# Kernel optimization log

Hardware: AMD Instinct MI355X
Metric: run time of the kernel (lower is better)

The kernel has to match this reference:

```python
import jax, jax.numpy as jnp
import numpy as np

B, N, M, C1, C2, H = 16, 4096, 1024, 256, 512, 256
SE_C = max(1, int(H / 24.0))  # 10
BN_EPS = 1e-5

def _bn(x, g, b):
    # training-mode BatchNorm over (B, n) per channel; x: [B, C, n]
    mean = jnp.mean(x, axis=(0, 2), keepdims=True)
    var = jnp.mean((x - mean) ** 2, axis=(0, 2), keepdims=True)  # biased var (torch)
    return (x - mean) * jax.lax.rsqrt(var + BN_EPS) * g[None, :, None] + b[None, :, None]

def _swish(x):
    return x * jax.nn.sigmoid(x)

def setup_inputs() -> dict:
    key = jax.random.key(0)
    ks = jax.random.split(key, 12)
    d = {
        "unknown": jax.random.normal(ks[0], (B, N, 3), jnp.float32),
        "known": jax.random.normal(ks[1], (B, M, 3), jnp.float32),
        "unknow_feats": jax.random.normal(ks[2], (B, C1, N), jnp.float32),
        "known_feats": jax.random.normal(ks[3], (B, C2, M), jnp.float32),
        # conv1 (C1+C2 -> H), no bias (bn)
        "W1": jax.random.normal(ks[4], (H, C1 + C2), jnp.float32) * (1.0 / np.sqrt(C1 + C2)),
        "g1": jnp.ones((H,), jnp.float32),
        "b1": jnp.zeros((H,), jnp.float32),
        # SE block (1x1 convs with bias, no pooling in this impl)
        "se_rw": jax.random.normal(ks[5], (SE_C, H), jnp.float32) * (1.0 / np.sqrt(H)),
        "se_rb": jnp.zeros((SE_C,), jnp.float32),
        "se_ew": jax.random.normal(ks[6], (H, SE_C), jnp.float32) * (1.0 / np.sqrt(SE_C)),
        "se_eb": jnp.zeros((H,), jnp.float32),
        # conv2 (H -> H), no bias
        "W2": jax.random.normal(ks[7], (H, H), jnp.float32) * (1.0 / np.sqrt(H)),
        "g2": jnp.ones((H,), jnp.float32),
        "b2": jnp.zeros((H,), jnp.float32),
    }
    return d

def reference(unknown, known, unknow_feats, known_feats,
              W1, g1, b1, se_rw, se_rb, se_ew, se_eb, W2, g2, b2):
    # three_nn: squared distances of each unknown point to all known points
    d2 = jnp.sum((unknown[:, :, None, :] - known[:, None, :, :]) ** 2, axis=-1)  # [B,N,M]
    neg_d, idx = jax.lax.top_k(-d2, 3)  # 3 smallest
    dist = -neg_d                                       # [B,N,3]
    dist_recip = 1.0 / (dist + 1e-8)
    weight = dist_recip / jnp.sum(dist_recip, axis=2, keepdims=True)  # [B,N,3]
    # three_interpolate: gather known_feats at idx, inverse-distance weighted sum
    gathered = jnp.take_along_axis(known_feats[:, :, None, :], idx[:, None, :, :], axis=3)  # [B,C2,N,3]
    interp = jnp.sum(gathered * weight[:, None, :, :], axis=-1)  # [B,C2,N]
    x = jnp.concatenate([interp, unknow_feats], axis=1)  # [B,C1+C2,N]
    # conv1 (1x1) + BN + SE
    h = jnp.einsum('oc,bcn->bon', W1, x)
    h = _bn(h, g1, b1)
    s = jnp.einsum('oc,bcn->bon', se_rw, h) + se_rb[None, :, None]
    s = _swish(s)
    s = jnp.einsum('oc,bcn->bon', se_ew, s) + se_eb[None, :, None]
    h = jax.nn.sigmoid(s) * h
    # conv2 (1x1) + BN + ReLU
    h = jnp.einsum('oc,bcn->bon', W2, h)
    h = _bn(h, g2, b2)
    return jax.nn.relu(h)  # [B, H, N]
```

## Files before the change

kernel.cpp:

```cpp
#include <hip/hip_runtime.h>
#include <math.h>

#define B_ 16
#define N_ 4096
#define M_ 1024
#define C1_ 256
#define C2_ 512
#define H_ 256
#define SEC_ 10
#define OC_ 8
#define BN_EPS 1e-5f

typedef _Float16 f16;
typedef f16 f16x8 __attribute__((ext_vector_type(8)));
typedef f16 f16x4 __attribute__((ext_vector_type(4)));
typedef f16 f16x2 __attribute__((ext_vector_type(2)));
typedef float f32x4 __attribute__((ext_vector_type(4)));

__global__ __launch_bounds__(256)
void three_nn_kernel(const float* __restrict__ unknown, const float* __restrict__ known,
                     int* __restrict__ idxp, float* __restrict__ wgtp)
{
    __shared__ float kx[M_], ky[M_], kz[M_];
    __shared__ float cd[4][64][3];
    __shared__ int   ci[4][64][3];
    const int b  = blockIdx.y;
    const int bn = blockIdx.x * 64;
    const int t  = threadIdx.x;
    const float* kb = known + (long)b * M_ * 3;

    {
        const float4 q0 = *(const float4*)(kb + 12*t);
        const float4 q1 = *(const float4*)(kb + 12*t + 4);
        const float4 q2 = *(const float4*)(kb + 12*t + 8);
        const int m = 4*t;
        kx[m+0]=q0.x; ky[m+0]=q0.y; kz[m+0]=q0.z;
        kx[m+1]=q0.w; ky[m+1]=q1.x; kz[m+1]=q1.y;
        kx[m+2]=q1.z; ky[m+2]=q1.w; kz[m+2]=q2.x;
        kx[m+3]=q2.y; ky[m+3]=q2.z; kz[m+3]=q2.w;
    }
    __syncthreads();

    const int w = t >> 6, ln = t & 63;
    const int n = bn + ln;
    const float* up = unknown + ((long)b * N_ + n) * 3;
    const float ux = up[0], uy = up[1], uz = up[2];

    float b0 = 1e30f, b1v = 1e30f, b2v = 1e30f;
    int j0 = 0, j1 = 0, j2 = 0;

    const int m0 = w * 256;
    for (int m = m0; m < m0 + 256; m += 4) {
        const float4 X = *(const float4*)&kx[m];
        const float4 Y = *(const float4*)&ky[m];
        const float4 Z = *(const float4*)&kz[m];
        const float px[4] = {X.x, X.y, X.z, X.w};
        const float py[4] = {Y.x, Y.y, Y.z, Y.w};
        const float pz[4] = {Z.x, Z.y, Z.z, Z.w};
        #pragma unroll
        for (int q = 0; q < 4; q++) {
            const float dx = ux - px[q], dy = uy - py[q], dz = uz - pz[q];
            const float d = dx*dx + dy*dy + dz*dz;
            if (d < b2v) {
                const int mm = m + q;
                if (d < b1v) {
                    b2v = b1v; j2 = j1;
                    if (d < b0) { b1v = b0; j1 = j0; b0 = d; j0 = mm; }
                    else        { b1v = d;  j1 = mm; }
                } else { b2v = d; j2 = mm; }
            }
        }
    }
    cd[w][ln][0] = b0;  cd[w][ln][1] = b1v; cd[w][ln][2] = b2v;
    ci[w][ln][0] = j0;  ci[w][ln][1] = j1;  ci[w][ln][2] = j2;
    __syncthreads();

    if (t < 64) {
        float d0 = cd[0][t][0], d1 = cd[0][t][1], d2 = cd[0][t][2];
        int   i0 = ci[0][t][0], i1 = ci[0][t][1], i2 = ci[0][t][2];
        #pragma unroll
        for (int c = 1; c < 4; c++) {
            #pragma unroll
            for (int j = 0; j < 3; j++) {
                const float d = cd[c][t][j];
                const int  ix = ci[c][t][j];
                if (d < d2) {
                    if (d < d1) {
                        d2 = d1; i2 = i1;
                        if (d < d0) { d1 = d0; i1 = i0; d0 = d; i0 = ix; }
                        else        { d1 = d;  i1 = ix; }
                    } else { d2 = d; i2 = ix; }
                }
            }
        }
        const float r0 = 1.f/(d0 + 1e-8f), r1 = 1.f/(d1 + 1e-8f), r2 = 1.f/(d2 + 1e-8f);
        const float rs = 1.f/(r0 + r1 + r2);
        const long base = ((long)b * N_ + bn + t) * 3;
        idxp[base+0] = i0; idxp[base+1] = i1; idxp[base+2] = i2;
        wgtp[base+0] = r0*rs; wgtp[base+1] = r1*rs; wgtp[base+2] = r2*rs;
    }
}

__global__ __launch_bounds__(256)
void convert_w_kernel(const float* __restrict__ W1, const float* __restrict__ W2,
                      f16* __restrict__ Wf0, f16* __restrict__ Wf1, f16* __restrict__ Wf2)
{
    const int which = blockIdx.y;
    const int K8    = (which == 0) ? 64 : 32;
    const int lda   = (which == 2) ? 256 : 768;
    const float* src = (which == 0) ? W1 : (which == 1) ? (W1 + 512) : W2;
    f16* dst = (which == 0) ? Wf0 : (which == 1) ? Wf1 : Wf2;
    const int t = blockIdx.x * 256 + threadIdx.x;
    const int total = 16 * K8 * 16;
    if (t >= total) return;
    const int l16 = t & 15;
    const int fi  = t >> 4;
    const int k8  = fi & (K8 - 1);
    const int rb  = fi >> ((which == 0) ? 6 : 5);
    const float* s = src + (long)(rb*16 + l16)*lda + k8*8;
    const float4 a = *(const float4*)s;
    const float4 c = *(const float4*)(s + 4);
    f16x8 h;
    h[0]=(f16)a.x; h[1]=(f16)a.y; h[2]=(f16)a.z; h[3]=(f16)a.w;
    h[4]=(f16)c.x; h[5]=(f16)c.y; h[6]=(f16)c.z; h[7]=(f16)c.w;
    *(f16x8*)&dst[(long)t*8] = h;
}

template<int MODE>
__global__ __launch_bounds__(256)
void gemm_mfma(const f16* __restrict__ Af, int K,
               const float* __restrict__ Bf, const f16* __restrict__ Bh,
               long strideB, int ldb,
               f16* __restrict__ Ch, long strideC, int ldc,
               const f16* __restrict__ Gt,
               const int* __restrict__ idxp, const float* __restrict__ wgtp,
               float* __restrict__ psum,
               const float* __restrict__ spart, const float* __restrict__ rbAdj,
               const float* __restrict__ se_ewp, const float* __restrict__ se_ebp,
               const float* __restrict__ a1p, const float* __restrict__ c1p)
{
    __shared__ __align__(16) char smem[64*264*2];
    __shared__ float sswl[SEC_*64];
    f16* const BsA = (f16*)smem;
    f16* const BsB = (f16*)(smem + 64*72*2);

    const int b   = blockIdx.z;
    const int bn  = blockIdx.x * 64;
    const int tid = threadIdx.x;
    const int l = tid & 63, w = tid >> 6;
    const int lane16 = l & 15, quad = l >> 4;
    const int K8 = K >> 3;

    const float* Bfb = nullptr;
    const f16*   Bhb = nullptr;
    if constexpr (MODE == 2) Bhb = Bh + (long)b*strideB;
    else                     Bfb = Bf + (long)b*strideB;

    if constexpr (MODE == 2) {
        for (int i = tid; i < SEC_*64; i += 256) {
            const int j = i >> 6, nn = i & 63;
            float v = rbAdj[j];
            #pragma unroll
            for (int oc = 0; oc < OC_; oc++)
                v += spart[(((long)oc*B_ + b)*SEC_ + j)*N_ + bn + nn];
            sswl[j*64 + nn] = v / (1.f + __expf(-v));
        }
        __syncthreads();
    }

    f32x4 acc[4][4];
    #pragma unroll
    for (int i = 0; i < 4; i++)
        #pragma unroll
        for (int j = 0; j < 4; j++)
            acc[i][j] = (f32x4){0.f, 0.f, 0.f, 0.f};

    auto stageB = [&](int k0, f16* __restrict__ Bsb) {
        #pragma unroll
        for (int it = 0; it < 2; it++) {
            const int slot = it*256 + tid;
            const int k2 = slot >> 4;
            const int n0 = (slot & 15) * 4;
            if constexpr (MODE == 2) {
                const int ka = k0 + 2*k2;
                const f16* s0 = Bhb + (long)ka*ldb + bn + n0;
                const f16x4 ua = *(const f16x4*)s0;
                const f16x4 ub = *(const f16x4*)(s0 + ldb);
                float val[2][4];
                #pragma unroll
                for (int r = 0; r < 2; r++) {
                    const int kr = ka + r;
                    const float aa = a1p[kr], cc = c1p[kr], eb = se_ebp[kr];
                    const float* ew = se_ewp + kr*SEC_;
                    #pragma unroll
                    for (int j = 0; j < 4; j++) {
                        float e = eb;
                        #pragma unroll
                        for (int q = 0; q < SEC_; q++) e += ew[q]*sswl[q*64 + n0 + j];
                        const float g  = 1.f/(1.f + __expf(-e));
                        const float hv = (r == 0) ? (float)ua[j] : (float)ub[j];
                        val[r][j] = g * (aa*hv + cc);
                    }
                }
                #pragma unroll
                for (int j = 0; j < 4; j++) {
                    f16x2 p; p[0] = (f16)val[0][j]; p[1] = (f16)val[1][j];
                    *(f16x2*)&Bsb[(n0+j)*72 + 2*k2] = p;
                }
            } else {
                const float* s0 = Bfb + (long)(k0 + 2*k2)*ldb + bn + n0;
                const float4 u = *(const float4*)s0;
                const float4 v = *(const float4*)(s0 + ldb);
                f16x2 p0, p1, p2, p3;
                p0[0]=(f16)u.x; p0[1]=(f16)v.x;
                p1[0]=(f16)u.y; p1[1]=(f16)v.y;
                p2[0]=(f16)u.z; p2[1]=(f16)v.z;
                p3[0]=(f16)u.w; p3[1]=(f16)v.w;
                *(f16x2*)&Bsb[(n0+0)*72 + 2*k2] = p0;
                *(f16x2*)&Bsb[(n0+1)*72 + 2*k2] = p1;
                *(f16x2*)&Bsb[(n0+2)*72 + 2*k2] = p2;
                *(f16x2*)&Bsb[(n0+3)*72 + 2*k2] = p3;
            }
        }
    };

    const f16* Afp = Af + quad*128 + lane16*8;
    const int bbase = lane16*72 + quad*8;

    stageB(0, BsA);
    __syncthreads();

    const int NKT = K >> 6;
    int cur = 0;
    for (int kt = 0; kt < NKT; kt++) {
        f16* const Bcur = cur ? BsB : BsA;
        if (kt + 1 < NKT) stageB((kt+1) << 6, cur ? BsA : BsB);
        #pragma unroll
        for (int s = 0; s < 2; s++) {
            const int ks = kt*2 + s;
            f16x8 af[4], bf[4];
            #pragma unroll
            for (int i = 0; i < 4; i++)
                af[i] = *(const f16x8*)(Afp + (long)((w*4 + i)*K8 + ks*4)*128);
            #pragma unroll
            for (int j = 0; j < 4; j++)
                bf[j] = *(const f16x8*)&Bcur[bbase + j*1152 + s*32];
            #pragma unroll
            for (int i = 0; i < 4; i++)
                #pragma unroll
                for (int j = 0; j < 4; j++)
                    acc[i][j] = __builtin_amdgcn_mfma_f32_16x16x32_f16(af[i], bf[j], acc[i][j], 0, 0, 0);
        }
        __syncthreads();
        cur ^= 1;
    }

    if constexpr (MODE == 0) {
        f16* Gl = (f16*)smem;
        #pragma unroll
        for (int i = 0; i < 4; i++)
            #pragma unroll
            for (int r = 0; r < 4; r++) {
                const int h = w*64 + i*16 + quad*4 + r;
                #pragma unroll
                for (int j = 0; j < 4; j++)
                    Gl[(j*16 + lane16)*264 + h] = (f16)acc[i][j][r];
            }
        __syncthreads();
        f16* Gtb = Ch + (long)b*strideC + (long)bn*H_;
        #pragma unroll
        for (int it = 0; it < 8; it++) {
            const int t = it*256 + tid;
            const int m = t >> 5, c = (t & 31)*8;
            *(f16x8*)&Gtb[m*H_ + c] = *(const f16x8*)&Gl[m*264 + c];
        }
    } else {
        if constexpr (MODE == 1) {
            f16* P = (f16*)smem;
            const int p  = tid >> 2;
            const int qd = tid & 3;
            const long ib = ((long)b*N_ + bn + p)*3;
            const int i0 = idxp[ib], i1 = idxp[ib+1], i2 = idxp[ib+2];
            const float w0 = wgtp[ib], w1 = wgtp[ib+1], w2 = wgtp[ib+2];
            const f16* gb = Gt + (long)b*M_*H_;
            const f16* g0 = gb + (long)i0*H_ + qd*64;
            const f16* g1 = gb + (long)i1*H_ + qd*64;
            const f16* g2 = gb + (long)i2*H_ + qd*64;
            f16* Pr = P + p*264 + qd*64;
            #pragma unroll
            for (int c = 0; c < 64; c += 8) {
                const f16x8 x0 = *(const f16x8*)&g0[c];
                const f16x8 x1 = *(const f16x8*)&g1[c];
                const f16x8 x2 = *(const f16x8*)&g2[c];
                f16x8 o;
                #pragma unroll
                for (int e = 0; e < 8; e++)
                    o[e] = (f16)(w0*(float)x0[e] + w1*(float)x1[e] + w2*(float)x2[e]);
                *(f16x8*)&Pr[c] = o;
            }
            __syncthreads();
            f16* P2 = (f16*)smem;
            #pragma unroll
            for (int i = 0; i < 4; i++)
                #pragma unroll
                for (int r = 0; r < 4; r++) {
                    const int h = w*64 + i*16 + quad*4 + r;
                    #pragma unroll
                    for (int j = 0; j < 4; j++)
                        acc[i][j][r] += (float)P2[(j*16 + lane16)*264 + h];
                }
        }
        const int bid = blockIdx.z * gridDim.x + blockIdx.x;
        float* ps = psum + (long)bid * (2*H_);
        f16* Cb = Ch + (long)b*strideC;
        #pragma unroll
        for (int i = 0; i < 4; i++)
            #pragma unroll
            for (int r = 0; r < 4; r++) {
                const int row = w*64 + i*16 + quad*4 + r;
                float s1 = 0.f, s2 = 0.f;
                #pragma unroll
                for (int j = 0; j < 4; j++) {
                    const float v = acc[i][j][r];
                    s1 += v; s2 += v*v;
                    Cb[(long)row*ldc + bn + j*16 + lane16] = (f16)v;
                }
                #pragma unroll
                for (int off = 1; off < 16; off <<= 1) {
                    s1 += __shfl_xor(s1, off, 64);
                    s2 += __shfl_xor(s2, off, 64);
                }
                if (lane16 == 0) {
                    ps[row]      = s1;
                    ps[H_ + row] = s2;
                }
            }
    }
}

__global__ __launch_bounds__(256)
void reduce_stats_kernel(const float* __restrict__ psum, float* __restrict__ stats, int nblk)
{
    __shared__ float red[8][33];
    const int o  = blockIdx.x*32 + (threadIdx.x & 31);
    const int ch = threadIdx.x >> 5;
    float s = 0.f;
    for (int bid = ch; bid < nblk; bid += 8)
        s += psum[(long)bid*(2*H_) + o];
    red[ch][threadIdx.x & 31] = s;
    __syncthreads();
    if (ch == 0) {
        float t = 0.f;
        #pragma unroll
        for (int c = 0; c < 8; c++) t += red[c][threadIdx.x & 31];
        stats[o] = t;
    }
}

__global__ __launch_bounds__(256)
void finalize1_kernel(const float* __restrict__ stats,
                      const float* __restrict__ g, const float* __restrict__ bb,
                      const float* __restrict__ se_rw, const float* __restrict__ se_rb,
                      float* __restrict__ a1, float* __restrict__ c1,
                      float* __restrict__ rw2, float* __restrict__ rbAdj)
{
    __shared__ float cbuf[H_];
    __shared__ float red[256];
    const int o = threadIdx.x;
    const float inv = 1.f / (float)(B_ * N_);
    const float S1 = stats[o], S2 = stats[H_ + o];
    const float mean = S1 * inv;
    const float var  = S2 * inv - mean*mean;
    const float a = g[o] * rsqrtf(var + BN_EPS);
    const float c = bb[o] - mean*a;
    a1[o] = a; c1[o] = c; cbuf[o] = c;
    for (int j = 0; j < SEC_; j++) rw2[j*H_ + o] = se_rw[j*H_ + o] * a;
    __syncthreads();
    for (int j = 0; j < SEC_; j++) {
        red[o] = se_rw[j*H_ + o] * cbuf[o];
        __syncthreads();
        for (int s = 128; s > 0; s >>= 1) {
            if (o < s) red[o] += red[o + s];
            __syncthreads();
        }
        if (o == 0) rbAdj[j] = se_rb[j] + red[0];
        __syncthreads();
    }
}

__global__ __launch_bounds__(256)
void se_reduce_kernel(const f16* __restrict__ h1h, const float* __restrict__ rw2,
                      float* __restrict__ spart)
{
    constexpr int OCH = H_ / OC_;
    __shared__ float rwl[SEC_][OCH];
    const int b = blockIdx.y, oc = blockIdx.z;
    const int n0 = blockIdx.x*1024 + threadIdx.x*4;
    for (int i = threadIdx.x; i < SEC_*OCH; i += 256)
        rwl[i/OCH][i%OCH] = rw2[(i/OCH)*H_ + oc*OCH + (i%OCH)];
    __syncthreads();
    f32x4 acc[SEC_];
    #pragma unroll
    for (int j = 0; j < SEC_; j++) acc[j] = (f32x4){0.f,0.f,0.f,0.f};
    const f16* hp = h1h + ((long)b*H_ + oc*OCH)*N_ + n0;
    for (int o = 0; o < OCH; o++) {
        const f16x4 h = *(const f16x4*)(hp + (long)o*N_);
        f32x4 hf; hf[0]=(float)h[0]; hf[1]=(float)h[1]; hf[2]=(float)h[2]; hf[3]=(float)h[3];
        #pragma unroll
        for (int j = 0; j < SEC_; j++) acc[j] += rwl[j][o]*hf;
    }
    #pragma unroll
    for (int j = 0; j < SEC_; j++)
        *(f32x4*)&spart[(((long)oc*B_ + b)*SEC_ + j)*N_ + n0] = acc[j];
}

__global__ __launch_bounds__(256)
void finalize2_kernel(const float* __restrict__ stats,
                      const float* __restrict__ g, const float* __restrict__ bb,
                      float* __restrict__ a2, float* __restrict__ c2)
{
    const int o = threadIdx.x;
    const float inv = 1.f / (float)(B_ * N_);
    const float S1 = stats[o], S2 = stats[H_ + o];
    const float mean = S1 * inv;
    const float var  = S2 * inv - mean*mean;
    const float a = g[o] * rsqrtf(var + BN_EPS);
    a2[o] = a; c2[o] = bb[o] - mean*a;
}

__global__ __launch_bounds__(256)
void bn_relu_kernel(const f16* __restrict__ h2h, float* __restrict__ out,
                    const float* __restrict__ a2, const float* __restrict__ c2)
{
    const long e = ((long)blockIdx.x*256 + threadIdx.x)*8;
    const int o = (int)((e >> 12) & (H_ - 1));
    const f16x8 v = *(const f16x8*)(h2h + e);
    const float a = a2[o], c = c2[o];
    float4 r0, r1;
    r0.x = fmaxf(a*(float)v[0] + c, 0.f);
    r0.y = fmaxf(a*(float)v[1] + c, 0.f);
    r0.z = fmaxf(a*(float)v[2] + c, 0.f);
    r0.w = fmaxf(a*(float)v[3] + c, 0.f);
    r1.x = fmaxf(a*(float)v[4] + c, 0.f);
    r1.y = fmaxf(a*(float)v[5] + c, 0.f);
    r1.z = fmaxf(a*(float)v[6] + c, 0.f);
    r1.w = fmaxf(a*(float)v[7] + c, 0.f);
    *(float4*)(out + e)     = r0;
    *(float4*)(out + e + 4) = r1;
}

extern "C" void kernel_launch(void* const* d_in, const int* in_sizes, int n_in,
                              void* d_out, int out_size, void* d_ws, size_t ws_size,
                              hipStream_t stream)
{
    const float* unknown = (const float*)d_in[0];
    const float* known   = (const float*)d_in[1];
    const float* uf      = (const float*)d_in[2];
    const float* kf      = (const float*)d_in[3];
    const float* W1      = (const float*)d_in[4];
    const float* g1      = (const float*)d_in[5];
    const float* b1      = (const float*)d_in[6];
    const float* se_rw   = (const float*)d_in[7];
    const float* se_rb   = (const float*)d_in[8];
    const float* se_ew   = (const float*)d_in[9];
    const float* se_eb   = (const float*)d_in[10];
    const float* W2      = (const float*)d_in[11];
    const float* g2      = (const float*)d_in[12];
    const float* b2      = (const float*)d_in[13];

    char* ws = (char*)d_ws;
    size_t off = 0;
    auto alloc = [&](size_t bytes) -> void* {
        void* p = ws + off;
        off += (bytes + 255) & ~(size_t)255;
        return p;
    };
    const int NBLK = (N_/64) * B_;
    int*   idxp   = (int*)  alloc((size_t)B_*N_*3*4);
    float* wgtp   = (float*)alloc((size_t)B_*N_*3*4);
    f16*   Gt     = (f16*)  alloc((size_t)B_*M_*H_*2);
    f16*   h1h    = (f16*)  alloc((size_t)B_*H_*N_*2);
    f16*   h2h    = (f16*)  alloc((size_t)B_*H_*N_*2);
    float* spart  = (float*)alloc((size_t)OC_*B_*SEC_*N_*4);
    float* psum1  = (float*)alloc((size_t)NBLK*2*H_*4);
    float* psum2  = (float*)alloc((size_t)NBLK*2*H_*4);
    float* stats1 = (float*)alloc(2*H_*4);
    float* stats2 = (float*)alloc(2*H_*4);
    float* a1     = (float*)alloc(H_*4);
    float* c1     = (float*)alloc(H_*4);
    float* rw2    = (float*)alloc(SEC_*H_*4);
    float* rbAdj  = (float*)alloc(64*4);
    float* a2     = (float*)alloc(H_*4);
    float* c2     = (float*)alloc(H_*4);
    f16*   Wf0    = (f16*)  alloc((size_t)H_*C2_*2);
    f16*   Wf1    = (f16*)  alloc((size_t)H_*C1_*2);
    f16*   Wf2    = (f16*)  alloc((size_t)H_*H_*2);
    (void)ws_size; (void)in_sizes; (void)n_in; (void)out_size;

    float* out = (float*)d_out;

    convert_w_kernel<<<dim3(64, 3), 256, 0, stream>>>(W1, W2, Wf0, Wf1, Wf2);

    three_nn_kernel<<<dim3(N_/64, B_), 256, 0, stream>>>(unknown, known, idxp, wgtp);

    gemm_mfma<0><<<dim3(M_/64, 1, B_), 256, 0, stream>>>(
        Wf0, C2_, kf, nullptr, (long)C2_*M_, M_,
        Gt, (long)M_*H_, 0,
        nullptr, nullptr, nullptr, nullptr,
        nullptr, nullptr, nullptr, nullptr, nullptr, nullptr);

    gemm_mfma<1><<<dim3(N_/64, 1, B_), 256, 0, stream>>>(
        Wf1, C1_, uf, nullptr, (long)C1_*N_, N_,
        h1h, (long)H_*N_, N_,
        Gt, idxp, wgtp, psum1,
        nullptr, nullptr, nullptr, nullptr, nullptr, nullptr);

    reduce_stats_kernel<<<dim3(16), 256, 0, stream>>>(psum1, stats1, NBLK);

    finalize1_kernel<<<1, 256, 0, stream>>>(stats1, g1, b1, se_rw, se_rb, a1, c1, rw2, rbAdj);

    se_reduce_kernel<<<dim3(N_/1024, B_, OC_), 256, 0, stream>>>(h1h, rw2, spart);

    gemm_mfma<2><<<dim3(N_/64, 1, B_), 256, 0, stream>>>(
        Wf2, H_, nullptr, h1h, (long)H_*N_, N_,
        h2h, (long)H_*N_, N_,
        nullptr, nullptr, nullptr, psum2,
        spart, rbAdj, se_ew, se_eb, a1, c1);

    reduce_stats_kernel<<<dim3(16), 256, 0, stream>>>(psum2, stats2, NBLK);

    finalize2_kernel<<<1, 256, 0, stream>>>(stats2, g2, b2, a2, c2);

    bn_relu_kernel<<<dim3((unsigned)((long)B_*H_*N_/2048)), 256, 0, stream>>>(h2h, out, a2, c2);
}
```

Baseline: 408.4 us.

## Stage full K-extent B tile in LDS up front with register prefetch, then run MFMA loop

The GEMM kernel takes K as a template parameter and loads the entire B panel (all K tiles) into shared memory before any MFMA work. Loads use two register buffers so each tile's global fetch overlaps the conversion and store of the previous one. The per-tile double-buffer barriers go away, and in mode 2 the first loads are issued before the SE pre-pass. In exchange, LDS use grows with K: 64 KB for the K=512 launch, which may cut occupancy, and the load phase no longer overlaps with MFMA compute.

```diff
diff --git a/kernel.cpp b/kernel.cpp
--- a/kernel.cpp
+++ b/kernel.cpp
@@ -126,9 +126,9 @@
     *(f16x8*)&dst[(long)t*8] = h;
 }
 
-template<int MODE>
-__global__ __launch_bounds__(256)
-void gemm_mfma(const f16* __restrict__ Af, int K,
+template<int MODE, int K>
+__global__ __launch_bounds__(256)
+void gemm_mfma(const f16* __restrict__ Af,
                const float* __restrict__ Bf, const f16* __restrict__ Bh,
                long strideB, int ldb,
                f16* __restrict__ Ch, long strideC, int ldc,
@@ -139,34 +139,27 @@
                const float* __restrict__ se_ewp, const float* __restrict__ se_ebp,
                const float* __restrict__ a1p, const float* __restrict__ c1p)
 {
-    __shared__ __align__(16) char smem[64*264*2];
+    constexpr int NKT  = K / 64;
+    constexpr int TILE = 64 * 72;
+    constexpr int EPIL = 64 * 264;
+    constexpr int SMEMH = (NKT*TILE > EPIL) ? NKT*TILE : EPIL;
+    __shared__ __align__(16) f16 smem[SMEMH];
     __shared__ float sswl[SEC_*64];
-    f16* const BsA = (f16*)smem;
-    f16* const BsB = (f16*)(smem + 64*72*2);
+    f16* const Bs = smem;
 
     const int b   = blockIdx.z;
     const int bn  = blockIdx.x * 64;
     const int tid = threadIdx.x;
     const int l = tid & 63, w = tid >> 6;
     const int lane16 = l & 15, quad = l >> 4;
-    const int K8 = K >> 3;
 
     const float* Bfb = nullptr;
     const f16*   Bhb = nullptr;
     if constexpr (MODE == 2) Bhb = Bh + (long)b*strideB;
     else                     Bfb = Bf + (long)b*strideB;
 
-    if constexpr (MODE == 2) {
-        for (int i = tid; i < SEC_*64; i += 256) {
-            const int j = i >> 6, nn = i & 63;
-            float v = rbAdj[j];
-            #pragma unroll
-            for (int oc = 0; oc < OC_; oc++)
-                v += spart[(((long)oc*B_ + b)*SEC_ + j)*N_ + bn + nn];
-            sswl[j*64 + nn] = v / (1.f + __expf(-v));
-        }
-        __syncthreads();
-    }
+    const int k2a = tid >> 4;
+    const int n0  = (tid & 15) * 4;
 
     f32x4 acc[4][4];
     #pragma unroll
@@ -175,21 +168,25 @@
         for (int j = 0; j < 4; j++)
             acc[i][j] = (f32x4){0.f, 0.f, 0.f, 0.f};
 
-    auto stageB = [&](int k0, f16* __restrict__ Bsb) {
-        #pragma unroll
-        for (int it = 0; it < 2; it++) {
-            const int slot = it*256 + tid;
-            const int k2 = slot >> 4;
-            const int n0 = (slot & 15) * 4;
-            if constexpr (MODE == 2) {
-                const int ka = k0 + 2*k2;
-                const f16* s0 = Bhb + (long)ka*ldb + bn + n0;
-                const f16x4 ua = *(const f16x4*)s0;
-                const f16x4 ub = *(const f16x4*)(s0 + ldb);
+    if constexpr (MODE == 2) {
+        auto LOADT = [&](int kt, f16x4* r) {
+            const f16* s0 = Bhb + (long)(kt*64 + 2*k2a)*ldb + bn + n0;
+            r[0] = *(const f16x4*)s0;
+            r[1] = *(const f16x4*)(s0 + ldb);
+            const f16* s1 = s0 + 32*(long)ldb;
+            r[2] = *(const f16x4*)s1;
+            r[3] = *(const f16x4*)(s1 + ldb);
+        };
+        auto STORET = [&](int kt, const f16x4* r) {
+            f16* dst = Bs + kt*TILE + n0*72 + 2*k2a;
+            #pragma unroll
+            for (int half = 0; half < 2; half++) {
+                const int ka = kt*64 + 2*k2a + 32*half;
+                const f16x4 ua = r[2*half], ub = r[2*half+1];
                 float val[2][4];
                 #pragma unroll
-                for (int r = 0; r < 2; r++) {
-                    const int kr = ka + r;
+                for (int rr = 0; rr < 2; rr++) {
+                    const int kr = ka + rr;
                     const float aa = a1p[kr], cc = c1p[kr], eb = se_ebp[kr];
                     const float* ew = se_ewp + kr*SEC_;
                     #pragma unroll
@@ -198,65 +195,93 @@
                         #pragma unroll
                         for (int q = 0; q < SEC_; q++) e += ew[q]*sswl[q*64 + n0 + j];
                         const float g  = 1.f/(1.f + __expf(-e));
-                        const float hv = (r == 0) ? (float)ua[j] : (float)ub[j];
-                        val[r][j] = g * (aa*hv + cc);
+                        const float hv = (rr == 0) ? (float)ua[j] : (float)ub[j];
+                        val[rr][j] = g * (aa*hv + cc);
                     }
                 }
                 #pragma unroll
                 for (int j = 0; j < 4; j++) {
                     f16x2 p; p[0] = (f16)val[0][j]; p[1] = (f16)val[1][j];
-                    *(f16x2*)&Bsb[(n0+j)*72 + 2*k2] = p;
-                }
-            } else {
-                const float* s0 = Bfb + (long)(k0 + 2*k2)*ldb + bn + n0;
-                const float4 u = *(const float4*)s0;
-                const float4 v = *(const float4*)(s0 + ldb);
+                    *(f16x2*)&dst[j*72 + 32*half] = p;
+                }
+            }
+        };
+        f16x4 ra[4], rb[4];
+        LOADT(0, ra);
+        LOADT(1, rb);
+        for (int i = tid; i < SEC_*64; i += 256) {
+            const int j = i >> 6, nn = i & 63;
+            float v = rbAdj[j];
+            #pragma unroll
+            for (int oc = 0; oc < OC_; oc++)
+                v += spart[(((long)oc*B_ + b)*SEC_ + j)*N_ + bn + nn];
+            sswl[j*64 + nn] = v / (1.f + __expf(-v));
+        }
+        __syncthreads();
+        #pragma unroll
+        for (int kt = 0; kt < NKT; kt++) {
+            f16x4* rc = (kt & 1) ? rb : ra;
+            STORET(kt, rc);
+            if (kt + 2 < NKT) LOADT(kt+2, rc);
+        }
+    } else {
+        auto LOADT = [&](int kt, float4* r) {
+            const float* s0 = Bfb + (long)(kt*64 + 2*k2a)*ldb + bn + n0;
+            r[0] = *(const float4*)s0;
+            r[1] = *(const float4*)(s0 + ldb);
+            const float* s1 = s0 + 32*(long)ldb;
+            r[2] = *(const float4*)s1;
+            r[3] = *(const float4*)(s1 + ldb);
+        };
+        auto STORET = [&](int kt, const float4* r) {
+            f16* dst = Bs + kt*TILE + n0*72 + 2*k2a;
+            #pragma unroll
+            for (int half = 0; half < 2; half++) {
+                const float4 u = r[2*half], v = r[2*half+1];
                 f16x2 p0, p1, p2, p3;
                 p0[0]=(f16)u.x; p0[1]=(f16)v.x;
                 p1[0]=(f16)u.y; p1[1]=(f16)v.y;
                 p2[0]=(f16)u.z; p2[1]=(f16)v.z;
                 p3[0]=(f16)u.w; p3[1]=(f16)v.w;
-                *(f16x2*)&Bsb[(n0+0)*72 + 2*k2] = p0;
-                *(f16x2*)&Bsb[(n0+1)*72 + 2*k2] = p1;
-                *(f16x2*)&Bsb[(n0+2)*72 + 2*k2] = p2;
-                *(f16x2*)&Bsb[(n0+3)*72 + 2*k2] = p3;
-            }
-        }
-    };
+                *(f16x2*)&dst[0*72 + 32*half] = p0;
+                *(f16x2*)&dst[1*72 + 32*half] = p1;
+                *(f16x2*)&dst[2*72 + 32*half] = p2;
+                *(f16x2*)&dst[3*72 + 32*half] = p3;
+            }
+        };
+        float4 ra[4], rb[4];
+        LOADT(0, ra);
+        LOADT(1, rb);
+        #pragma unroll
+        for (int kt = 0; kt < NKT; kt++) {
+            float4* rc = (kt & 1) ? rb : ra;
+            STORET(kt, rc);
+            if (kt + 2 < NKT) LOADT(kt+2, rc);
+        }
+    }
+    __syncthreads();
 
     const f16* Afp = Af + quad*128 + lane16*8;
     const int bbase = lane16*72 + quad*8;
-
-    stageB(0, BsA);
-    __syncthreads();
-
-    const int NKT = K >> 6;
-    int cur = 0;
-    for (int kt = 0; kt < NKT; kt++) {
-        f16* const Bcur = cur ? BsB : BsA;
-        if (kt + 1 < NKT) stageB((kt+1) << 6, cur ? BsA : BsB);
-        #pragma unroll
-        for (int s = 0; s < 2; s++) {
-            const int ks = kt*2 + s;
-            f16x8 af[4], bf[4];
-            #pragma unroll
-            for (int i = 0; i < 4; i++)
-                af[i] = *(const f16x8*)(Afp + (long)((w*4 + i)*K8 + ks*4)*128);
+    #pragma unroll
+    for (int s = 0; s < 2*NKT; s++) {
+        f16x8 af[4], bf[4];
+        #pragma unroll
+        for (int i = 0; i < 4; i++)
+            af[i] = *(const f16x8*)(Afp + (long)((w*4 + i)*(K/8) + s*4)*128);
+        #pragma unroll
+        for (int j = 0; j < 4; j++)
+            bf[j] = *(const f16x8*)&Bs[(s>>1)*TILE + bbase + j*1152 + (s&1)*32];
+        #pragma unroll
+        for (int i = 0; i < 4; i++)
             #pragma unroll
             for (int j = 0; j < 4; j++)
-                bf[j] = *(const f16x8*)&Bcur[bbase + j*1152 + s*32];
-            #pragma unroll
-            for (int i = 0; i < 4; i++)
-                #pragma unroll
-                for (int j = 0; j < 4; j++)
-                    acc[i][j] = __builtin_amdgcn_mfma_f32_16x16x32_f16(af[i], bf[j], acc[i][j], 0, 0, 0);
-        }
+                acc[i][j] = __builtin_amdgcn_mfma_f32_16x16x32_f16(af[i], bf[j], acc[i][j], 0, 0, 0);
+    }
+
+    if constexpr (MODE == 0) {
         __syncthreads();
-        cur ^= 1;
-    }
-
-    if constexpr (MODE == 0) {
-        f16* Gl = (f16*)smem;
+        f16* Gl = smem;
         #pragma unroll
         for (int i = 0; i < 4; i++)
             #pragma unroll
@@ -276,7 +301,8 @@
         }
     } else {
         if constexpr (MODE == 1) {
-            f16* P = (f16*)smem;
+            __syncthreads();
+            f16* P = smem;
             const int p  = tid >> 2;
             const int qd = tid & 3;
             const long ib = ((long)b*N_ + bn + p)*3;
@@ -299,7 +325,6 @@
                 *(f16x8*)&Pr[c] = o;
             }
             __syncthreads();
-            f16* P2 = (f16*)smem;
             #pragma unroll
             for (int i = 0; i < 4; i++)
                 #pragma unroll
@@ -307,7 +332,7 @@
                     const int h = w*64 + i*16 + quad*4 + r;
                     #pragma unroll
                     for (int j = 0; j < 4; j++)
-                        acc[i][j][r] += (float)P2[(j*16 + lane16)*264 + h];
+                        acc[i][j][r] += (float)P[(j*16 + lane16)*264 + h];
                 }
         }
         const int bid = blockIdx.z * gridDim.x + blockIdx.x;
@@ -503,14 +528,14 @@
 
     three_nn_kernel<<<dim3(N_/64, B_), 256, 0, stream>>>(unknown, known, idxp, wgtp);
 
-    gemm_mfma<0><<<dim3(M_/64, 1, B_), 256, 0, stream>>>(
-        Wf0, C2_, kf, nullptr, (long)C2_*M_, M_,
+    gemm_mfma<0, C2_><<<dim3(M_/64, 1, B_), 256, 0, stream>>>(
+        Wf0, kf, nullptr, (long)C2_*M_, M_,
         Gt, (long)M_*H_, 0,
         nullptr, nullptr, nullptr, nullptr,
         nullptr, nullptr, nullptr, nullptr, nullptr, nullptr);
 
-    gemm_mfma<1><<<dim3(N_/64, 1, B_), 256, 0, stream>>>(
-        Wf1, C1_, uf, nullptr, (long)C1_*N_, N_,
+    gemm_mfma<1, C1_><<<dim3(N_/64, 1, B_), 256, 0, stream>>>(
+        Wf1, uf, nullptr, (long)C1_*N_, N_,
         h1h, (long)H_*N_, N_,
         Gt, idxp, wgtp, psum1,
         nullptr, nullptr, nullptr, nullptr, nullptr, nullptr);
@@ -521,8 +546,8 @@
 
     se_reduce_kernel<<<dim3(N_/1024, B_, OC_), 256, 0, stream>>>(h1h, rw2, spart);
 
-    gemm_mfma<2><<<dim3(N_/64, 1, B_), 256, 0, stream>>>(
-        Wf2, H_, nullptr, h1h, (long)H_*N_, N_,
+    gemm_mfma<2, H_><<<dim3(N_/64, 1, B_), 256, 0, stream>>>(
+        Wf2, nullptr, h1h, (long)H_*N_, N_,
         h2h, (long)H_*N_, N_,
         nullptr, nullptr, nullptr, psum2,
         spart, rbAdj, se_ew, se_eb, a1, c1);
```

Result: no change. 413.7 us (+1.3%).
